# Kernel optimization log

Hardware: AMD Instinct MI355X
Metric: run time of the kernel (lower is better)

Reference implementation:

```python
import jax, jax.numpy as jnp
import numpy as np

N_NODES = 100000

def gcn_conv(h, row, col, w, W, b, n):
    # linear transform then symmetric-normalized weighted aggregation (PyG GCNConv)
    h = h @ W                                   # [N, F_out]
    deg = jax.ops.segment_sum(w, row, num_segments=n)          # weighted in-degree [N]
    dinv = jnp.where(deg > 0, jax.lax.rsqrt(deg), 0.0)
    norm = dinv[row] * w * dinv[col]            # [E]
    msg = norm[:, None] * h[col]                # gather+scale, [E, F_out]
    return jax.ops.segment_sum(msg, row, num_segments=n) + b

def setup_inputs() -> dict:
    key = jax.random.key(0)
    ks = jax.random.split(key, 6)
    N, E, D, H = N_NODES, 1600000, 128, 128
    x = jax.random.normal(ks[0], (N, D), dtype=jnp.float32)
    edge_index = jax.random.randint(ks[1], (2, E), 0, N, dtype=jnp.int64)
    edge_weight = jax.random.uniform(ks[2], (E,), dtype=jnp.float32)
    W1 = jax.random.normal(ks[3], (D, H), dtype=jnp.float32) / np.sqrt(D)
    b1 = jnp.zeros((H,), dtype=jnp.float32)
    W2 = jax.random.normal(ks[4], (H, H), dtype=jnp.float32) / np.sqrt(H)
    b2 = jnp.zeros((H,), dtype=jnp.float32)
    return {"x": x, "edge_index": edge_index, "edge_weight": edge_weight,
            "W1": W1, "b1": b1, "W2": W2, "b2": b2}

def reference(x, edge_index, edge_weight, W1, b1, W2, b2):
    n = x.shape[0]
    # add self-loops with weight 1 (PyG gcn_norm default)
    loops = jnp.arange(n, dtype=edge_index.dtype)
    row = jnp.concatenate([edge_index[0], loops])
    col = jnp.concatenate([edge_index[1], loops])
    w = jnp.concatenate([edge_weight, jnp.ones((n,), dtype=edge_weight.dtype)])
    h = gcn_conv(x, row, col, w, W1, b1, n)
    h = jax.nn.relu(h)  # dropout is identity in eval mode
    h = gcn_conv(h, row, col, w, W2, b2, n)
    return h
```

## Files before the change

### kernel.cpp

```cpp
#include <hip/hip_runtime.h>


constexpr int N_NODES = 100000;
constexpr int FD = 128;
constexpr int NPAD = 100352;
constexpr int CAP = 48;
constexpr int PSH = 7;
constexpr int PROWS = 128;
constexpr int NP = (N_NODES + PROWS - 1) / PROWS;
constexpr int RCAP = 2560;
constexpr int PSTRIDE = 16;
constexpr int EPB = 4096;
constexpr int EPT = 16;

typedef __attribute__((ext_vector_type(8))) short bf16x8;
typedef __attribute__((ext_vector_type(4))) float f32x4;
#define MFMA16(a, b, c) __builtin_amdgcn_mfma_f32_16x16x32_bf16(a, b, c, 0, 0, 0)

static __device__ __forceinline__ unsigned f2bf(float x) {
  unsigned u = __float_as_uint(x);
  return (u + 0x7FFFu + ((u >> 16) & 1u)) >> 16;
}
static __device__ __forceinline__ float bflo(unsigned u) {
  return __uint_as_float(u << 16);
}
static __device__ __forceinline__ float bfhi(unsigned u) {
  return __uint_as_float(u & 0xFFFF0000u);
}

__global__ __launch_bounds__(256) void k_part(const int* __restrict__ row,
                                              const int* __restrict__ col,
                                              const float* __restrict__ w,
                                              int* __restrict__ pcnt,
                                              int2* __restrict__ rec, int E) {
  __shared__ int lcnt[NP];
  const int t = threadIdx.x;
  const int e0 = blockIdx.x * EPB;
  for (int p = t; p < NP; p += 256) lcnt[p] = 0;
  __syncthreads();

  int packed[EPT];
  int cols[EPT];
  int ws[EPT];
#pragma unroll
  for (int i = 0; i < EPT; i++) {
    int e = e0 + i * 256 + t;
    packed[i] = -1;
    if (e < E) {
      int r = row[e];
      cols[i] = col[e];
      ws[i] = __float_as_int(w[e]);
      int part = r >> PSH, rl = r & (PROWS - 1);
      int off = atomicAdd(&lcnt[part], 1);
      packed[i] = part | (rl << 10) | (off << 17);
    }
  }
  __syncthreads();

  for (int p = t; p < NP; p += 256) {
    int c = lcnt[p];
    int base = 0;
    if (c) base = atomicAdd(&pcnt[p * PSTRIDE], c);
    lcnt[p] = base;
  }
  __syncthreads();

#pragma unroll
  for (int i = 0; i < EPT; i++) {
    int pk = packed[i];
    if (pk >= 0) {
      int part = pk & 0x3FF;
      int rl = (pk >> 10) & 0x7F;
      int pos = lcnt[part] + (pk >> 17);
      if (pos < RCAP)
        rec[(size_t)part * RCAP + pos] = make_int2(cols[i] | (rl << 20), ws[i]);
    }
  }
}

__global__ __launch_bounds__(256) void k_bin(const int* __restrict__ pcnt,
                                             const int2* __restrict__ rec,
                                             int2* __restrict__ bucket,
                                             int* __restrict__ cnt,
                                             float* __restrict__ dinv) {
  __shared__ int lcnt[PROWS];
  __shared__ float lsum[PROWS];
  const int part = blockIdx.x, t = threadIdx.x;
  if (t < PROWS) { lcnt[t] = 0; lsum[t] = 0.f; }
  __syncthreads();
  const int n = min(pcnt[part * PSTRIDE], RCAP);
  const int row0 = part << PSH;
  const int2* rp = rec + (size_t)part * RCAP;
  for (int j = t; j < n; j += 256) {
    int2 R = rp[j];
    int rl = R.x >> 20;
    int c = R.x & 0xFFFFF;
    int p = atomicAdd(&lcnt[rl], 1);
    if (p < CAP) bucket[(size_t)(row0 + rl) * CAP + p] = make_int2(c, R.y);
    atomicAdd(&lsum[rl], __int_as_float(R.y));
  }
  __syncthreads();
  int i = row0 + t;
  if (t < PROWS && i < N_NODES) {
    cnt[i] = min(lcnt[t], CAP);
    dinv[i] = rsqrtf(lsum[t] + 1.0f);
  }
}

__global__ __launch_bounds__(128) void k_prep(const float* __restrict__ W,
                                              ushort* __restrict__ WhT,
                                              ushort* __restrict__ WlT) {
  int n0 = blockIdx.x;
  int k = threadIdx.x;
  float v = W[k * FD + n0];
  unsigned h = f2bf(v);
  float r = v - bflo(h);
  WhT[n0 * FD + k] = (ushort)h;
  WlT[n0 * FD + k] = (ushort)f2bf(r);
}

__global__ __launch_bounds__(512) void k_gemm(const float* __restrict__ X,
                                              const ushort* __restrict__ WhT,
                                              const ushort* __restrict__ WlT,
                                              ushort* __restrict__ Yb,
                                              int relu_in) {
  __shared__ ushort sl[32768];
  ushort* lwh = sl;
  ushort* lwl = sl + 16384;
  const int t = threadIdx.x;
  const int wid = t >> 6;
  const int lane = t & 63;
  const int g = lane >> 4;
  const int lr = lane & 15;

  const size_t row_base = (size_t)blockIdx.x * 128 + wid * 16 + lr;
  const size_t rowc = row_base < N_NODES ? row_base : 0;
  const float* xr = X + rowc * FD;
  float xv[4][8];
#pragma unroll
  for (int ks = 0; ks < 4; ks++) {
    *(float4*)&xv[ks][0] = *(const float4*)(xr + ks * 32 + g * 8);
    *(float4*)&xv[ks][4] = *(const float4*)(xr + ks * 32 + g * 8 + 4);
  }

  {
    const uint4* gh = (const uint4*)WhT;
    const uint4* gl = (const uint4*)WlT;
#pragma unroll
    for (int i = 0; i < 4; i++) {
      int idx = i * 512 + t;
      int byte = idx * 16;
      int n = byte >> 8;
      int swz = byte ^ ((n & 7) << 4);
      *(uint4*)((char*)lwh + swz) = gh[idx];
      *(uint4*)((char*)lwl + swz) = gl[idx];
    }
  }
  __syncthreads();

  f32x4 acc[8];
#pragma unroll
  for (int nf = 0; nf < 8; nf++) acc[nf] = (f32x4)(0.f);

#pragma unroll
  for (int ks = 0; ks < 4; ks++) {
    bf16x8 a_h, a_l;
#pragma unroll
    for (int j = 0; j < 8; j++) {
      float v = xv[ks][j];
      if (relu_in) v = fmaxf(v, 0.f);
      unsigned hb_ = f2bf(v);
      float r = v - bflo(hb_);
      a_h[j] = (short)hb_;
      a_l[j] = (short)f2bf(r);
    }
#pragma unroll
    for (int nf = 0; nf < 8; nf++) {
      int n = nf * 16 + lr;
      int byte = n * 256 + ks * 64 + g * 16;
      int swz = byte ^ ((n & 7) << 4);
      bf16x8 bh = *(const bf16x8*)((const char*)lwh + swz);
      bf16x8 bl = *(const bf16x8*)((const char*)lwl + swz);
      acc[nf] = MFMA16(a_h, bh, acc[nf]);
      acc[nf] = MFMA16(a_l, bh, acc[nf]);
      acc[nf] = MFMA16(a_h, bl, acc[nf]);
    }
  }

  __syncthreads();
#pragma unroll
  for (int nf = 0; nf < 8; nf++) {
#pragma unroll
    for (int r = 0; r < 4; r++) {
      int rl = wid * 16 + g * 4 + r;
      int byte = rl * 256 + (nf * 16 + lr) * 2;
      int swz = byte ^ ((rl & 7) << 4);
      *(ushort*)((char*)sl + swz) = (ushort)f2bf(acc[nf][r]);
    }
  }
  __syncthreads();
#pragma unroll
  for (int i = 0; i < 4; i++) {
    int idx = i * 512 + t;
    int byte = idx * 16;
    int rl = byte >> 8;
    int swz = byte ^ ((rl & 7) << 4);
    uint4 v = *(const uint4*)((const char*)sl + swz);
    size_t rg = (size_t)blockIdx.x * 128 + rl;
    if (rg < N_NODES) *(uint4*)(Yb + rg * FD + ((byte & 255) >> 1)) = v;
  }
}

static __device__ __forceinline__ void acc8(float* a, float s, uint4 g) {
  a[0] += s * bflo(g.x);
  a[1] += s * bfhi(g.x);
  a[2] += s * bflo(g.y);
  a[3] += s * bfhi(g.y);
  a[4] += s * bflo(g.z);
  a[5] += s * bfhi(g.z);
  a[6] += s * bflo(g.w);
  a[7] += s * bfhi(g.w);
}

__global__ __launch_bounds__(256, 4) void k_gather(
    const ushort* __restrict__ hb, const int* __restrict__ cnt,
    const int2* __restrict__ bucket, const float* __restrict__ dinv,
    const float* __restrict__ b, float* __restrict__ out) {
  int t = blockIdx.x * 256 + threadIdx.x;
  int i = t >> 4, q = t & 15;
  if (i >= N_NODES) return;
  float di = dinv[i];
  const uint4* H = (const uint4*)hb;
  uint4 hv = H[(size_t)i * 16 + q];
  float a[8];
  a[0] = di * bflo(hv.x); a[1] = di * bfhi(hv.x);
  a[2] = di * bflo(hv.y); a[3] = di * bfhi(hv.y);
  a[4] = di * bflo(hv.z); a[5] = di * bfhi(hv.z);
  a[6] = di * bflo(hv.w); a[7] = di * bfhi(hv.w);
  const int c = min(cnt[i], CAP);
  const int2* bk = bucket + (size_t)i * CAP;
  const int nb = (c + 7) >> 3;

  int2 cur[8];
  if (nb > 0) {
#pragma unroll
    for (int j = 0; j < 4; j++)
      *(int4*)&cur[j * 2] = *(const int4*)&bk[j * 2];
  }
  for (int bt = 0; bt < nb; bt++) {
    int2 nxt[8];
    if (bt + 1 < nb) {
#pragma unroll
      for (int j = 0; j < 4; j++)
        *(int4*)&nxt[j * 2] = *(const int4*)&bk[(bt + 1) * 8 + j * 2];
    }
    const int base = bt * 8;
    int idx[8];
    float wv[8];
#pragma unroll
    for (int j = 0; j < 8; j++) {
      bool v = (base + j) < c;
      idx[j] = v ? cur[j].x : i;
      wv[j] = v ? __int_as_float(cur[j].y) : 0.f;
    }
    uint4 g[8];
#pragma unroll
    for (int j = 0; j < 8; j++) g[j] = H[(size_t)idx[j] * 16 + q];
    float s[8];
#pragma unroll
    for (int j = 0; j < 8; j++) s[j] = wv[j] * dinv[idx[j]];
#pragma unroll
    for (int j = 0; j < 8; j++) acc8(a, s[j], g[j]);
#pragma unroll
    for (int j = 0; j < 8; j++) cur[j] = nxt[j];
  }
  float4 b0 = ((const float4*)b)[q * 2];
  float4 b1 = ((const float4*)b)[q * 2 + 1];
  float* o = out + (size_t)i * FD + q * 8;
  float4 o0, o1;
  o0.x = di * a[0] + b0.x; o0.y = di * a[1] + b0.y;
  o0.z = di * a[2] + b0.z; o0.w = di * a[3] + b0.w;
  o1.x = di * a[4] + b1.x; o1.y = di * a[5] + b1.y;
  o1.z = di * a[6] + b1.z; o1.w = di * a[7] + b1.w;
  ((float4*)o)[0] = o0;
  ((float4*)o)[1] = o1;
}

extern "C" void kernel_launch(void* const* d_in, const int* in_sizes, int n_in,
                              void* d_out, int out_size, void* d_ws, size_t ws_size,
                              hipStream_t stream) {
  const float* x  = (const float*)d_in[0];
  const int*   ei = (const int*)d_in[1];
  const float* ew = (const float*)d_in[2];
  const float* W1 = (const float*)d_in[3];
  const float* b1 = (const float*)d_in[4];
  const float* W2 = (const float*)d_in[5];
  const float* b2 = (const float*)d_in[6];
  float* out = (float*)d_out;

  const int E = in_sizes[2];
  const int* row = ei;
  const int* col = ei + E;

  int*    pcnt   = (int*)d_ws;
  float*  dinv   = (float*)(pcnt + 16384);
  int*    cnt    = (int*)(dinv + NPAD);
  int2*   bucket = (int2*)(cnt + NPAD);
  int2*   rec    = bucket + (size_t)NPAD * CAP;
  ushort* hb     = (ushort*)(rec + (size_t)NP * RCAP);
  ushort* w1ht   = hb + (size_t)N_NODES * FD;
  ushort* w1lt   = w1ht + FD * FD;
  ushort* w2ht   = w1lt + FD * FD;
  ushort* w2lt   = w2ht + FD * FD;

  hipMemsetAsync(pcnt, 0, 16384 * sizeof(int), stream);
  k_prep<<<FD, FD, 0, stream>>>(W1, w1ht, w1lt);
  k_prep<<<FD, FD, 0, stream>>>(W2, w2ht, w2lt);
  const int part_grid = (E + EPB - 1) / EPB;
  k_part<<<part_grid, 256, 0, stream>>>(row, col, ew, pcnt, rec, E);
  k_bin<<<NP, 256, 0, stream>>>(pcnt, rec, bucket, cnt, dinv);

  const int gemm_grid = (N_NODES + 127) / 128;
  const int ga_grid   = (N_NODES * 16 + 255) / 256;

  k_gemm<<<gemm_grid, 512, 0, stream>>>(x, w1ht, w1lt, hb, 0);
  k_gather<<<ga_grid, 256, 0, stream>>>(hb, cnt, bucket, dinv, b1, out);
  k_gemm<<<gemm_grid, 512, 0, stream>>>(out, w2ht, w2lt, hb, 1);
  k_gather<<<ga_grid, 256, 0, stream>>>(hb, cnt, bucket, dinv, b2, out);
}
```

Before: 336.0 us.

## Fold source-side dinv into GEMM epilogue and software-pipeline gather loads

The GEMM epilogue now multiplies each output row by dinv[row] before bf16 conversion. The gather kernel therefore no longer loads dinv for every neighbor, which removes one random global access per edge. The gather loop is also restructured to issue the next batch's feature loads before accumulating the current batch, with sched_barrier to keep that order. This raises register pressure from the double-buffered g arrays and changes where bf16 rounding happens relative to the scaling.

Measured after the change: 545.6 us. +62.4%, slower.

```diff
diff --git a/kernel.cpp b/kernel.cpp
--- a/kernel.cpp
+++ b/kernel.cpp
@@ -122,6 +122,7 @@
 __global__ __launch_bounds__(512) void k_gemm(const float* __restrict__ X,
                                               const ushort* __restrict__ WhT,
                                               const ushort* __restrict__ WlT,
+                                              const float* __restrict__ dinv,
                                               ushort* __restrict__ Yb,
                                               int relu_in) {
   __shared__ ushort sl[32768];
@@ -187,6 +188,8 @@
     }
   }
 
+  float4 dv = *(const float4*)&dinv[blockIdx.x * 128 + wid * 16 + g * 4];
+
   __syncthreads();
 #pragma unroll
   for (int nf = 0; nf < 8; nf++) {
@@ -195,7 +198,7 @@
       int rl = wid * 16 + g * 4 + r;
       int byte = rl * 256 + (nf * 16 + lr) * 2;
       int swz = byte ^ ((rl & 7) << 4);
-      *(ushort*)((char*)sl + swz) = (ushort)f2bf(acc[nf][r]);
+      *(ushort*)((char*)sl + swz) = (ushort)f2bf(acc[nf][r] * (&dv.x)[r]);
     }
   }
   __syncthreads();
@@ -233,46 +236,58 @@
   const uint4* H = (const uint4*)hb;
   uint4 hv = H[(size_t)i * 16 + q];
   float a[8];
-  a[0] = di * bflo(hv.x); a[1] = di * bfhi(hv.x);
-  a[2] = di * bflo(hv.y); a[3] = di * bfhi(hv.y);
-  a[4] = di * bflo(hv.z); a[5] = di * bfhi(hv.z);
-  a[6] = di * bflo(hv.w); a[7] = di * bfhi(hv.w);
+  a[0] = bflo(hv.x); a[1] = bfhi(hv.x);
+  a[2] = bflo(hv.y); a[3] = bfhi(hv.y);
+  a[4] = bflo(hv.z); a[5] = bfhi(hv.z);
+  a[6] = bflo(hv.w); a[7] = bfhi(hv.w);
   const int c = min(cnt[i], CAP);
   const int2* bk = bucket + (size_t)i * CAP;
   const int nb = (c + 7) >> 3;
 
-  int2 cur[8];
+  int2 nxt[8];
+  uint4 g[8];
+  float wv[8];
   if (nb > 0) {
-#pragma unroll
-    for (int j = 0; j < 4; j++)
-      *(int4*)&cur[j * 2] = *(const int4*)&bk[j * 2];
+    int2 cur[8];
+#pragma unroll
+    for (int j = 0; j < 4; j++) *(int4*)&cur[j * 2] = *(const int4*)&bk[j * 2];
+#pragma unroll
+    for (int j = 0; j < 8; j++) {
+      bool v = j < c;
+      int idx = v ? cur[j].x : i;
+      wv[j] = v ? __int_as_float(cur[j].y) : 0.f;
+      g[j] = H[(size_t)idx * 16 + q];
+    }
+#pragma unroll
+    for (int j = 0; j < 4; j++) *(int4*)&nxt[j * 2] = *(const int4*)&bk[8 + j * 2];
+    __builtin_amdgcn_sched_barrier(0);
   }
   for (int bt = 0; bt < nb; bt++) {
-    int2 nxt[8];
-    if (bt + 1 < nb) {
-#pragma unroll
-      for (int j = 0; j < 4; j++)
-        *(int4*)&nxt[j * 2] = *(const int4*)&bk[(bt + 1) * 8 + j * 2];
-    }
-    const int base = bt * 8;
-    int idx[8];
-    float wv[8];
-#pragma unroll
-    for (int j = 0; j < 8; j++) {
-      bool v = (base + j) < c;
-      idx[j] = v ? cur[j].x : i;
-      wv[j] = v ? __int_as_float(cur[j].y) : 0.f;
-    }
-    uint4 g[8];
-#pragma unroll
-    for (int j = 0; j < 8; j++) g[j] = H[(size_t)idx[j] * 16 + q];
-    float s[8];
-#pragma unroll
-    for (int j = 0; j < 8; j++) s[j] = wv[j] * dinv[idx[j]];
-#pragma unroll
-    for (int j = 0; j < 8; j++) acc8(a, s[j], g[j]);
-#pragma unroll
-    for (int j = 0; j < 8; j++) cur[j] = nxt[j];
+    uint4 g2[8];
+    float wv2[8];
+    const bool more = (bt + 1) < nb;
+    if (more) {
+      const int base = (bt + 1) * 8;
+#pragma unroll
+      for (int j = 0; j < 8; j++) {
+        bool v = (base + j) < c;
+        int idx = v ? nxt[j].x : i;
+        wv2[j] = v ? __int_as_float(nxt[j].y) : 0.f;
+        g2[j] = H[(size_t)idx * 16 + q];
+      }
+      if (bt + 2 < nb) {
+#pragma unroll
+        for (int j = 0; j < 4; j++)
+          *(int4*)&nxt[j * 2] = *(const int4*)&bk[(bt + 2) * 8 + j * 2];
+      }
+      __builtin_amdgcn_sched_barrier(0);
+    }
+#pragma unroll
+    for (int j = 0; j < 8; j++) acc8(a, wv[j], g[j]);
+    if (more) {
+#pragma unroll
+      for (int j = 0; j < 8; j++) { g[j] = g2[j]; wv[j] = wv2[j]; }
+    }
   }
   float4 b0 = ((const float4*)b)[q * 2];
   float4 b1 = ((const float4*)b)[q * 2 + 1];
@@ -323,8 +338,8 @@
   const int gemm_grid = (N_NODES + 127) / 128;
   const int ga_grid   = (N_NODES * 16 + 255) / 256;
 
-  k_gemm<<<gemm_grid, 512, 0, stream>>>(x, w1ht, w1lt, hb, 0);
+  k_gemm<<<gemm_grid, 512, 0, stream>>>(x, w1ht, w1lt, dinv, hb, 0);
   k_gather<<<ga_grid, 256, 0, stream>>>(hb, cnt, bucket, dinv, b1, out);
-  k_gemm<<<gemm_grid, 512, 0, stream>>>(out, w2ht, w2lt, hb, 1);
+  k_gemm<<<gemm_grid, 512, 0, stream>>>(out, w2ht, w2lt, dinv, hb, 1);
   k_gather<<<ga_grid, 256, 0, stream>>>(hb, cnt, bucket, dinv, b2, out);
 }
```

## Pre-scale GEMM output by dinv and store hidden features in feature-sliced layout

Applied to the files above, without the earlier changes.

The GEMM epilogue now multiplies each output row by its dinv, so the gather no longer loads dinv for every neighbor index. The hidden feature buffer is rearranged into 8 column slices of 16 features, with each slice stored contiguously across nodes. The gather grid is organised so consecutive blocks in a group of 8 cover the same 128 nodes, one slice each, with 2 threads per node per slice. The aim is better L2 locality for random neighbor gathers, since each slice's working set is smaller. The cost is 8x more traversals of the bucket index lists, a larger padded buffer, and partial-line gathers of 32 bytes per node.

Result: slower. 405.5 us (+20.7%).

```diff
diff --git a/kernel.cpp b/kernel.cpp
--- a/kernel.cpp
+++ b/kernel.cpp
@@ -12,6 +12,7 @@
 constexpr int PSTRIDE = 16;
 constexpr int EPB = 4096;
 constexpr int EPT = 16;
+constexpr int NSL = 8;
 
 typedef __attribute__((ext_vector_type(8))) short bf16x8;
 typedef __attribute__((ext_vector_type(4))) float f32x4;
@@ -122,6 +123,7 @@
 __global__ __launch_bounds__(512) void k_gemm(const float* __restrict__ X,
                                               const ushort* __restrict__ WhT,
                                               const ushort* __restrict__ WlT,
+                                              const float* __restrict__ dinv,
                                               ushort* __restrict__ Yb,
                                               int relu_in) {
   __shared__ ushort sl[32768];
@@ -187,6 +189,8 @@
     }
   }
 
+  float4 dv = *(const float4*)&dinv[blockIdx.x * 128 + wid * 16 + g * 4];
+
   __syncthreads();
 #pragma unroll
   for (int nf = 0; nf < 8; nf++) {
@@ -195,7 +199,7 @@
       int rl = wid * 16 + g * 4 + r;
       int byte = rl * 256 + (nf * 16 + lr) * 2;
       int swz = byte ^ ((rl & 7) << 4);
-      *(ushort*)((char*)sl + swz) = (ushort)f2bf(acc[nf][r]);
+      *(ushort*)((char*)sl + swz) = (ushort)f2bf(acc[nf][r] * (&dv.x)[r]);
     }
   }
   __syncthreads();
@@ -207,7 +211,10 @@
     int swz = byte ^ ((rl & 7) << 4);
     uint4 v = *(const uint4*)((const char*)sl + swz);
     size_t rg = (size_t)blockIdx.x * 128 + rl;
-    if (rg < N_NODES) *(uint4*)(Yb + rg * FD + ((byte & 255) >> 1)) = v;
+    int cb = (byte & 255) >> 4;
+    int s = cb >> 1, qq = cb & 1;
+    if (rg < N_NODES)
+      *(uint4*)(Yb + (size_t)s * NPAD * 16 + rg * 16 + qq * 8) = v;
   }
 }
 
@@ -226,17 +233,20 @@
     const ushort* __restrict__ hb, const int* __restrict__ cnt,
     const int2* __restrict__ bucket, const float* __restrict__ dinv,
     const float* __restrict__ b, float* __restrict__ out) {
-  int t = blockIdx.x * 256 + threadIdx.x;
-  int i = t >> 4, q = t & 15;
+  const int s = blockIdx.x & (NSL - 1);
+  const int range = blockIdx.x >> 3;
+  const int t = threadIdx.x;
+  const int lrow = t >> 1, q = t & 1;
+  const int i = range * 128 + lrow;
   if (i >= N_NODES) return;
-  float di = dinv[i];
-  const uint4* H = (const uint4*)hb;
-  uint4 hv = H[(size_t)i * 16 + q];
+  const float di = dinv[i];
+  const uint4* Hs = (const uint4*)hb + (size_t)s * NPAD * 2;
+  uint4 hv = Hs[(size_t)i * 2 + q];
   float a[8];
-  a[0] = di * bflo(hv.x); a[1] = di * bfhi(hv.x);
-  a[2] = di * bflo(hv.y); a[3] = di * bfhi(hv.y);
-  a[4] = di * bflo(hv.z); a[5] = di * bfhi(hv.z);
-  a[6] = di * bflo(hv.w); a[7] = di * bfhi(hv.w);
+  a[0] = bflo(hv.x); a[1] = bfhi(hv.x);
+  a[2] = bflo(hv.y); a[3] = bfhi(hv.y);
+  a[4] = bflo(hv.z); a[5] = bfhi(hv.z);
+  a[6] = bflo(hv.w); a[7] = bfhi(hv.w);
   const int c = min(cnt[i], CAP);
   const int2* bk = bucket + (size_t)i * CAP;
   const int nb = (c + 7) >> 3;
@@ -265,18 +275,16 @@
     }
     uint4 g[8];
 #pragma unroll
-    for (int j = 0; j < 8; j++) g[j] = H[(size_t)idx[j] * 16 + q];
-    float s[8];
-#pragma unroll
-    for (int j = 0; j < 8; j++) s[j] = wv[j] * dinv[idx[j]];
-#pragma unroll
-    for (int j = 0; j < 8; j++) acc8(a, s[j], g[j]);
+    for (int j = 0; j < 8; j++) g[j] = Hs[(size_t)idx[j] * 2 + q];
+#pragma unroll
+    for (int j = 0; j < 8; j++) acc8(a, wv[j], g[j]);
 #pragma unroll
     for (int j = 0; j < 8; j++) cur[j] = nxt[j];
   }
-  float4 b0 = ((const float4*)b)[q * 2];
-  float4 b1 = ((const float4*)b)[q * 2 + 1];
-  float* o = out + (size_t)i * FD + q * 8;
+  const float* bp = b + s * 16 + q * 8;
+  float4 b0 = *(const float4*)bp;
+  float4 b1 = *(const float4*)(bp + 4);
+  float* o = out + (size_t)i * FD + s * 16 + q * 8;
   float4 o0, o1;
   o0.x = di * a[0] + b0.x; o0.y = di * a[1] + b0.y;
   o0.z = di * a[2] + b0.z; o0.w = di * a[3] + b0.w;
@@ -308,7 +316,7 @@
   int2*   bucket = (int2*)(cnt + NPAD);
   int2*   rec    = bucket + (size_t)NPAD * CAP;
   ushort* hb     = (ushort*)(rec + (size_t)NP * RCAP);
-  ushort* w1ht   = hb + (size_t)N_NODES * FD;
+  ushort* w1ht   = hb + (size_t)NPAD * FD;
   ushort* w1lt   = w1ht + FD * FD;
   ushort* w2ht   = w1lt + FD * FD;
   ushort* w2lt   = w2ht + FD * FD;
@@ -321,10 +329,10 @@
   k_bin<<<NP, 256, 0, stream>>>(pcnt, rec, bucket, cnt, dinv);
 
   const int gemm_grid = (N_NODES + 127) / 128;
-  const int ga_grid   = (N_NODES * 16 + 255) / 256;
-
-  k_gemm<<<gemm_grid, 512, 0, stream>>>(x, w1ht, w1lt, hb, 0);
+  const int ga_grid   = gemm_grid * NSL;
+
+  k_gemm<<<gemm_grid, 512, 0, stream>>>(x, w1ht, w1lt, dinv, hb, 0);
   k_gather<<<ga_grid, 256, 0, stream>>>(hb, cnt, bucket, dinv, b1, out);
-  k_gemm<<<gemm_grid, 512, 0, stream>>>(out, w2ht, w2lt, hb, 1);
+  k_gemm<<<gemm_grid, 512, 0, stream>>>(out, w2ht, w2lt, dinv, hb, 1);
   k_gather<<<ga_grid, 256, 0, stream>>>(hb, cnt, bucket, dinv, b2, out);
 }
```
